# Kernel tuning notes

Measured on AMD Instinct MI355X. Metric: run time of the kernel, lower is better.

## Reference

```python
import jax, jax.numpy as jnp
import numpy as np


def setup_inputs() -> dict:
    key = jax.random.key(0)
    x = jax.random.normal(key, (1024, 65536), dtype=jnp.float32)
    return {"x": x, "k": 64}


def reference(x, k):
    # BatchTopK: ReLU, then keep the k*batch largest activations across the
    # ENTIRE flattened batch, zeroing everything else.
    acts = jax.nn.relu(x)
    flat = acts.reshape(-1)                      # [batch * d_sae]
    k_total = k * x.shape[0]
    vals, idx = jax.lax.top_k(flat, k_total)     # global selection
    out = jnp.zeros_like(flat).at[idx].set(vals) # scatter back
    return out.reshape(acts.shape)
```

## Files before the change

### kernel.cpp

```cpp
#include <hip/hip_runtime.h>
#include <stdint.h>


#define HDR_CURSOR 0
#define HDR_FLAG   1
#define HDR_THR    2
#define HDR_ICUT   3
#define CAND_OFF   4096
#define LDS_STAGE  2048
#define ROWS       1024u
#define SPEC       3.0f

__global__ void k_init(uint32_t* hdr, uint32_t force_flag) {
  if (threadIdx.x < 64u) hdr[threadIdx.x] = 0u;
  if (threadIdx.x == 0u) hdr[HDR_FLAG] = force_flag;
}

__global__ __launch_bounds__(256) void k_compact(
    const float4* __restrict__ x4, const float* __restrict__ x,
    uint2* __restrict__ cand, uint32_t* __restrict__ hdr,
    uint32_t cap, uint32_t n4, uint32_t n) {
  __shared__ uint32_t s_cnt;
  __shared__ uint32_t s_base;
  __shared__ uint2 s_buf[LDS_STAGE];
  if (threadIdx.x == 0u) s_cnt = 0u;
  __syncthreads();

  uint32_t tid = blockIdx.x * blockDim.x + threadIdx.x;
  uint32_t stride = gridDim.x * blockDim.x;
  uint32_t n8 = n4 >> 1;
  for (uint32_t i = tid; i < n8; i += stride) {
    float4 a = x4[2u * i];
    float4 b = x4[2u * i + 1u];
    uint32_t gi = i * 8u;
    if (a.x >= SPEC) { uint32_t p = atomicAdd(&s_cnt, 1u); if (p < LDS_STAGE) s_buf[p] = make_uint2(__float_as_uint(a.x), gi); }
    if (a.y >= SPEC) { uint32_t p = atomicAdd(&s_cnt, 1u); if (p < LDS_STAGE) s_buf[p] = make_uint2(__float_as_uint(a.y), gi + 1u); }
    if (a.z >= SPEC) { uint32_t p = atomicAdd(&s_cnt, 1u); if (p < LDS_STAGE) s_buf[p] = make_uint2(__float_as_uint(a.z), gi + 2u); }
    if (a.w >= SPEC) { uint32_t p = atomicAdd(&s_cnt, 1u); if (p < LDS_STAGE) s_buf[p] = make_uint2(__float_as_uint(a.w), gi + 3u); }
    if (b.x >= SPEC) { uint32_t p = atomicAdd(&s_cnt, 1u); if (p < LDS_STAGE) s_buf[p] = make_uint2(__float_as_uint(b.x), gi + 4u); }
    if (b.y >= SPEC) { uint32_t p = atomicAdd(&s_cnt, 1u); if (p < LDS_STAGE) s_buf[p] = make_uint2(__float_as_uint(b.y), gi + 5u); }
    if (b.z >= SPEC) { uint32_t p = atomicAdd(&s_cnt, 1u); if (p < LDS_STAGE) s_buf[p] = make_uint2(__float_as_uint(b.z), gi + 6u); }
    if (b.w >= SPEC) { uint32_t p = atomicAdd(&s_cnt, 1u); if (p < LDS_STAGE) s_buf[p] = make_uint2(__float_as_uint(b.w), gi + 7u); }
  }
  uint32_t tail0 = n8 * 8u;
  if (blockIdx.x == 0u && threadIdx.x < (n - tail0)) {
    uint32_t gi = tail0 + threadIdx.x;
    float v = x[gi];
    if (v >= SPEC) { uint32_t p = atomicAdd(&s_cnt, 1u); if (p < LDS_STAGE) s_buf[p] = make_uint2(__float_as_uint(v), gi); }
  }
  __syncthreads();
  uint32_t cnt = s_cnt;
  if (cnt == 0u) return;
  uint32_t wcnt = cnt < (uint32_t)LDS_STAGE ? cnt : (uint32_t)LDS_STAGE;
  if (threadIdx.x == 0u) {
    s_base = atomicAdd(&hdr[HDR_CURSOR], cnt);
    if (cnt > (uint32_t)LDS_STAGE) atomicOr(&hdr[HDR_FLAG], 1u);
  }
  __syncthreads();
  uint32_t base = s_base;
  for (uint32_t j = threadIdx.x; j < wcnt; j += blockDim.x) {
    uint32_t g = base + j;
    if (g < cap) cand[g] = s_buf[j];
  }
  if (threadIdx.x == 0u && base + wcnt > cap) atomicOr(&hdr[HDR_FLAG], 1u);
}

__global__ __launch_bounds__(1024) void k_select(
    const uint2* __restrict__ cand, uint32_t* __restrict__ hdr,
    const int* __restrict__ kptr, uint32_t cap) {
  __shared__ uint32_t hist[2048];
  __shared__ uint32_t s_sel, s_rank, s_eqcnt, s_icut;
  __shared__ uint32_t eq_idx[4096];
  uint32_t tid = threadIdx.x;
  uint32_t K = (uint32_t)kptr[0] * ROWS;
  uint32_t M = hdr[HDR_CURSOR];
  if (hdr[HDR_FLAG] != 0u || M > cap || M < K) {
    if (tid == 0u) hdr[HDR_FLAG] = 1u;
    return;
  }
  if (K == 0u) {
    if (tid == 0u) { hdr[HDR_THR] = 0xFFFFFFFFu; hdr[HDR_ICUT] = 0xFFFFFFFFu; }
    return;
  }
  const uint4* __restrict__ cand4 = (const uint4*)cand;
  uint32_t M2 = M >> 1;
  uint32_t R = K;
  uint32_t prefix = 0u;
  for (int lvl = 0; lvl < 3; ++lvl) {
    uint32_t shift = (lvl == 0) ? 21u : (lvl == 1 ? 10u : 0u);
    uint32_t nb = (lvl == 2) ? 1024u : 2048u;
    for (uint32_t b = tid; b < nb; b += 1024u) hist[b] = 0u;
    __syncthreads();
    for (uint32_t j = tid; j < M2; j += 1024u) {
      uint4 c = cand4[j];
      uint32_t k0 = c.x, k1 = c.z;
      bool v0 = true, v1 = true;
      if (lvl == 1) { v0 = ((k0 >> 21) == prefix); v1 = ((k1 >> 21) == prefix); }
      if (lvl == 2) { v0 = ((k0 >> 10) == prefix); v1 = ((k1 >> 10) == prefix); }
      if (v0) atomicAdd(&hist[(k0 >> shift) & (nb - 1u)], 1u);
      if (v1) atomicAdd(&hist[(k1 >> shift) & (nb - 1u)], 1u);
    }
    if (tid == 0u && (M & 1u)) {
      uint32_t key = cand[M - 1u].x;
      bool v = true;
      if (lvl == 1) v = ((key >> 21) == prefix);
      if (lvl == 2) v = ((key >> 10) == prefix);
      if (v) atomicAdd(&hist[(key >> shift) & (nb - 1u)], 1u);
    }
    __syncthreads();
    if (tid < 64u) {
      uint32_t seg = nb >> 6;
      uint32_t base = tid * seg;
      uint32_t lanesum = 0u;
      for (uint32_t j = 0; j < seg; ++j) lanesum += hist[base + j];
      uint32_t s = lanesum;
      for (int d = 1; d < 64; d <<= 1) {
        uint32_t v = (uint32_t)__shfl_down((int)s, d, 64);
        if ((int)tid + d < 64) s += v;
      }
      uint32_t above = s - lanesum;
      if (above < R && above + lanesum >= R) {
        uint32_t r = R - above;
        uint32_t cum = 0u;
        for (int j = (int)seg - 1; j >= 0; --j) {
          uint32_t c = hist[base + (uint32_t)j];
          if (cum + c >= r) { s_sel = base + (uint32_t)j; s_rank = r - cum; break; }
          cum += c;
        }
      }
    }
    __syncthreads();
    uint32_t sel = s_sel;
    R = s_rank;
    if (lvl == 0) prefix = sel;
    else if (lvl == 1) prefix = (prefix << 11) | sel;
    else prefix = (prefix << 10) | sel;
  }
  uint32_t thr_key = prefix;
  uint32_t E = hist[thr_key & 1023u];
  uint32_t T = R;
  uint32_t icut = 0xFFFFFFFFu;
  if (T < E) {
    if (tid == 0u) { s_eqcnt = 0u; s_icut = 0xFFFFFFFFu; }
    __syncthreads();
    for (uint32_t i = tid; i < M; i += 1024u) {
      uint2 c = cand[i];
      if (c.x == thr_key) { uint32_t p = atomicAdd(&s_eqcnt, 1u); if (p < 4096u) eq_idx[p] = c.y; }
    }
    __syncthreads();
    if (s_eqcnt > 4096u) {
      if (tid == 0u) hdr[HDR_FLAG] = 1u;
      return;
    }
    uint32_t ec = s_eqcnt;
    for (uint32_t e = tid; e < ec; e += 1024u) {
      uint32_t me = eq_idx[e];
      uint32_t rank = 0u;
      for (uint32_t j = 0; j < ec; ++j) rank += (eq_idx[j] < me) ? 1u : 0u;
      if (rank == T - 1u) s_icut = me;
    }
    __syncthreads();
    icut = s_icut;
  }
  if (tid == 0u) { hdr[HDR_THR] = thr_key; hdr[HDR_ICUT] = icut; }
}

__global__ __launch_bounds__(256) void k_scatter(
    const uint2* __restrict__ cand, const uint32_t* __restrict__ hdr,
    float* __restrict__ out, uint32_t cap) {
  if (hdr[HDR_FLAG] != 0u) return;
  uint32_t M = hdr[HDR_CURSOR]; if (M > cap) M = cap;
  uint32_t thr = hdr[HDR_THR], icut = hdr[HDR_ICUT];
  uint32_t stride = gridDim.x * blockDim.x;
  for (uint32_t i = blockIdx.x * blockDim.x + threadIdx.x; i < M; i += stride) {
    uint2 c = cand[i];
    if (c.x > thr || (c.x == thr && c.y <= icut)) out[c.y] = __uint_as_float(c.x);
  }
}

__global__ __launch_bounds__(1024) void k_fallback(
    const float* __restrict__ x, float* __restrict__ out,
    const int* __restrict__ kptr, const uint32_t* __restrict__ hdr, uint32_t n) {
  if (hdr[HDR_FLAG] == 0u) return;
  __shared__ uint32_t hist[2048];
  __shared__ uint32_t s_sel, s_rank, s_found, s_eqcnt, s_icut;
  __shared__ uint32_t eq_idx[4096];
  uint32_t tid = threadIdx.x;
  uint32_t K = (uint32_t)kptr[0] * ROWS;
  uint32_t prefix = 0u;
  uint32_t R = K;
  bool zero_thr = (K == 0u);
  for (int lvl = 0; lvl < 3 && !zero_thr; ++lvl) {
    uint32_t shift = (lvl == 0) ? 21u : (lvl == 1 ? 10u : 0u);
    uint32_t nb = (lvl == 2) ? 1024u : 2048u;
    for (uint32_t b = tid; b < nb; b += 1024u) hist[b] = 0u;
    __syncthreads();
    for (uint32_t i = tid; i < n; i += 1024u) {
      float v = x[i];
      uint32_t key = (v > 0.f) ? __float_as_uint(v) : 0u;
      bool valid = (key != 0u);
      if (lvl == 1) valid = valid && ((key >> 21) == prefix);
      if (lvl == 2) valid = valid && ((key >> 10) == prefix);
      if (valid) atomicAdd(&hist[(key >> shift) & (nb - 1u)], 1u);
    }
    __syncthreads();
    if (tid == 0u) {
      uint32_t cum = 0u, sel = 0u, rr = R, found = 0u;
      for (int b = (int)nb - 1; b >= 0; --b) {
        uint32_t c = hist[b];
        if (cum + c >= R) { sel = (uint32_t)b; rr = R - cum; found = 1u; break; }
        cum += c;
      }
      s_sel = sel; s_rank = rr; s_found = found;
    }
    __syncthreads();
    if (s_found == 0u) {
      zero_thr = true;
    } else {
      uint32_t sel = s_sel;
      R = s_rank;
      if (lvl == 0) prefix = sel;
      else if (lvl == 1) prefix = (prefix << 11) | sel;
      else prefix = (prefix << 10) | sel;
    }
    __syncthreads();
  }
  uint32_t thr_key = zero_thr ? 0u : prefix;
  uint32_t icut = 0xFFFFFFFFu;
  if (!zero_thr) {
    uint32_t E = hist[thr_key & 1023u];
    uint32_t T = R;
    if (T < E) {
      if (tid == 0u) { s_eqcnt = 0u; s_icut = 0xFFFFFFFFu; }
      __syncthreads();
      for (uint32_t i = tid; i < n; i += 1024u) {
        float v = x[i];
        if (v > 0.f && __float_as_uint(v) == thr_key) {
          uint32_t p = atomicAdd(&s_eqcnt, 1u);
          if (p < 4096u) eq_idx[p] = i;
        }
      }
      __syncthreads();
      uint32_t ec = s_eqcnt < 4096u ? s_eqcnt : 4096u;
      for (uint32_t e = tid; e < ec; e += 1024u) {
        uint32_t me = eq_idx[e];
        uint32_t rank = 0u;
        for (uint32_t j = 0; j < ec; ++j) rank += (eq_idx[j] < me) ? 1u : 0u;
        if (rank == T - 1u) s_icut = me;
      }
      __syncthreads();
      icut = s_icut;
    }
  }
  for (uint32_t i = tid; i < n; i += 1024u) {
    float v = x[i];
    uint32_t key = (v > 0.f) ? __float_as_uint(v) : 0u;
    bool keep = (key > thr_key) || (key != 0u && key == thr_key && i <= icut);
    out[i] = keep ? v : 0.f;
  }
}

extern "C" void kernel_launch(void* const* d_in, const int* in_sizes, int n_in,
                              void* d_out, int out_size, void* d_ws, size_t ws_size,
                              hipStream_t stream) {
  const float* x = (const float*)d_in[0];
  const int* kptr = (const int*)d_in[1];
  float* out = (float*)d_out;
  uint32_t n = (uint32_t)in_sizes[0];
  uint32_t n4 = n >> 2;

  uint32_t* hdr = (uint32_t*)d_ws;
  uint2* cand = (uint2*)((char*)d_ws + CAND_OFF);
  uint32_t cap = (ws_size > (size_t)CAND_OFF) ? (uint32_t)((ws_size - CAND_OFF) / 8) : 0u;
  uint32_t force = (cap < 131072u) ? 1u : 0u;

  k_init<<<1, 64, 0, stream>>>(hdr, force);
  hipMemsetAsync(d_out, 0, (size_t)out_size * sizeof(float), stream);
  k_compact<<<2048, 256, 0, stream>>>((const float4*)x, x, cand, hdr, cap, n4, n);
  k_select<<<1, 1024, 0, stream>>>(cand, hdr, kptr, cap);
  k_fallback<<<1, 1024, 0, stream>>>(x, out, kptr, hdr, n);
  k_scatter<<<256, 256, 0, stream>>>(cand, hdr, out, cap);
}
```

Baseline: 569.1 us.

## Fuse output zeroing into candidate scan kernel with interleaved block roles

Replaces the separate hipMemsetAsync of the output with a combined kernel in which even blocks write zeros and odd blocks scan the input for candidates above the speculative threshold. Both memory streams can then run concurrently instead of back to back. The scan now reads one float4 per thread per iteration and uses a wavefront ballot to skip the atomic path when no lane has a candidate. The cost is a larger grid, and the zero-filling blocks keep the same shared-memory footprint and may compete for bandwidth with the scan.

```diff
diff --git a/kernel.cpp b/kernel.cpp
--- a/kernel.cpp
+++ b/kernel.cpp
@@ -16,34 +16,43 @@
   if (threadIdx.x == 0u) hdr[HDR_FLAG] = force_flag;
 }
 
-__global__ __launch_bounds__(256) void k_compact(
+__global__ __launch_bounds__(256) void k_zero_scan(
+    float4* __restrict__ out4, float* __restrict__ out,
     const float4* __restrict__ x4, const float* __restrict__ x,
     uint2* __restrict__ cand, uint32_t* __restrict__ hdr,
-    uint32_t cap, uint32_t n4, uint32_t n) {
+    uint32_t cap, uint32_t n4, uint32_t n, uint32_t half) {
+  uint32_t role = blockIdx.x & 1u;
+  uint32_t bid  = blockIdx.x >> 1;
+  uint32_t stride = half * 256u;
+  uint32_t tail0 = n4 * 4u;
+
+  if (role == 0u) {
+    const float4 z = make_float4(0.f, 0.f, 0.f, 0.f);
+    for (uint32_t i = bid * 256u + threadIdx.x; i < n4; i += stride)
+      out4[i] = z;
+    if (bid == 0u && threadIdx.x < (n - tail0))
+      out[tail0 + threadIdx.x] = 0.f;
+    return;
+  }
+
   __shared__ uint32_t s_cnt;
   __shared__ uint32_t s_base;
   __shared__ uint2 s_buf[LDS_STAGE];
   if (threadIdx.x == 0u) s_cnt = 0u;
   __syncthreads();
 
-  uint32_t tid = blockIdx.x * blockDim.x + threadIdx.x;
-  uint32_t stride = gridDim.x * blockDim.x;
-  uint32_t n8 = n4 >> 1;
-  for (uint32_t i = tid; i < n8; i += stride) {
-    float4 a = x4[2u * i];
-    float4 b = x4[2u * i + 1u];
-    uint32_t gi = i * 8u;
-    if (a.x >= SPEC) { uint32_t p = atomicAdd(&s_cnt, 1u); if (p < LDS_STAGE) s_buf[p] = make_uint2(__float_as_uint(a.x), gi); }
-    if (a.y >= SPEC) { uint32_t p = atomicAdd(&s_cnt, 1u); if (p < LDS_STAGE) s_buf[p] = make_uint2(__float_as_uint(a.y), gi + 1u); }
-    if (a.z >= SPEC) { uint32_t p = atomicAdd(&s_cnt, 1u); if (p < LDS_STAGE) s_buf[p] = make_uint2(__float_as_uint(a.z), gi + 2u); }
-    if (a.w >= SPEC) { uint32_t p = atomicAdd(&s_cnt, 1u); if (p < LDS_STAGE) s_buf[p] = make_uint2(__float_as_uint(a.w), gi + 3u); }
-    if (b.x >= SPEC) { uint32_t p = atomicAdd(&s_cnt, 1u); if (p < LDS_STAGE) s_buf[p] = make_uint2(__float_as_uint(b.x), gi + 4u); }
-    if (b.y >= SPEC) { uint32_t p = atomicAdd(&s_cnt, 1u); if (p < LDS_STAGE) s_buf[p] = make_uint2(__float_as_uint(b.y), gi + 5u); }
-    if (b.z >= SPEC) { uint32_t p = atomicAdd(&s_cnt, 1u); if (p < LDS_STAGE) s_buf[p] = make_uint2(__float_as_uint(b.z), gi + 6u); }
-    if (b.w >= SPEC) { uint32_t p = atomicAdd(&s_cnt, 1u); if (p < LDS_STAGE) s_buf[p] = make_uint2(__float_as_uint(b.w), gi + 7u); }
-  }
-  uint32_t tail0 = n8 * 8u;
-  if (blockIdx.x == 0u && threadIdx.x < (n - tail0)) {
+  for (uint32_t i = bid * 256u + threadIdx.x; i < n4; i += stride) {
+    float4 a = x4[i];
+    bool has = (a.x >= SPEC) || (a.y >= SPEC) || (a.z >= SPEC) || (a.w >= SPEC);
+    if (__ballot(has ? 1 : 0)) {
+      uint32_t gi = i * 4u;
+      if (a.x >= SPEC) { uint32_t p = atomicAdd(&s_cnt, 1u); if (p < LDS_STAGE) s_buf[p] = make_uint2(__float_as_uint(a.x), gi); }
+      if (a.y >= SPEC) { uint32_t p = atomicAdd(&s_cnt, 1u); if (p < LDS_STAGE) s_buf[p] = make_uint2(__float_as_uint(a.y), gi + 1u); }
+      if (a.z >= SPEC) { uint32_t p = atomicAdd(&s_cnt, 1u); if (p < LDS_STAGE) s_buf[p] = make_uint2(__float_as_uint(a.z), gi + 2u); }
+      if (a.w >= SPEC) { uint32_t p = atomicAdd(&s_cnt, 1u); if (p < LDS_STAGE) s_buf[p] = make_uint2(__float_as_uint(a.w), gi + 3u); }
+    }
+  }
+  if (bid == 0u && threadIdx.x < (n - tail0)) {
     uint32_t gi = tail0 + threadIdx.x;
     float v = x[gi];
     if (v >= SPEC) { uint32_t p = atomicAdd(&s_cnt, 1u); if (p < LDS_STAGE) s_buf[p] = make_uint2(__float_as_uint(v), gi); }
@@ -274,9 +283,10 @@
   uint32_t cap = (ws_size > (size_t)CAND_OFF) ? (uint32_t)((ws_size - CAND_OFF) / 8) : 0u;
   uint32_t force = (cap < 131072u) ? 1u : 0u;
 
+  const uint32_t HALF = 2048u;
   k_init<<<1, 64, 0, stream>>>(hdr, force);
-  hipMemsetAsync(d_out, 0, (size_t)out_size * sizeof(float), stream);
-  k_compact<<<2048, 256, 0, stream>>>((const float4*)x, x, cand, hdr, cap, n4, n);
+  k_zero_scan<<<2u * HALF, 256, 0, stream>>>((float4*)out, out, (const float4*)x, x,
+                                             cand, hdr, cap, n4, n, HALF);
   k_select<<<1, 1024, 0, stream>>>(cand, hdr, kptr, cap);
   k_fallback<<<1, 1024, 0, stream>>>(x, out, kptr, hdr, n);
   k_scatter<<<256, 256, 0, stream>>>(cand, hdr, out, cap);
```

New measurement: 563.1 us. No clear change (-1.1%).
